# Kernel tuning notes

Hardware: AMD Instinct MI355X
Metric: run time of the kernel (lower is better)

Reference implementation:

```python
import jax, jax.numpy as jnp
import numpy as np

R = 0.2                 # ball-query radius (Descriptor.r)
MAX_NBRS = 64           # CONFIG['Descriptor']['max_num_neighbors']


def setup_inputs() -> dict:
    key = jax.random.key(0)
    k1, k2, k3, k4, k5, k6 = jax.random.split(key, 6)
    N, F, M = 100000, 64, 2048
    x = jax.random.normal(k1, (N, F), dtype=jnp.float32)
    pos = jax.random.normal(k2, (N, 3), dtype=jnp.float32)
    batch = jnp.sort(jax.random.randint(k3, (N,), 0, 4, dtype=jnp.int64))
    key_idx = jax.random.randint(k4, (M,), 0, N, dtype=jnp.int64)
    # MLP params: Linear(F+3 -> 128), ReLU, Linear(128 -> 128)
    H = 128
    W1 = jax.random.normal(k5, (F + 3, H), dtype=jnp.float32) / np.sqrt(F + 3)
    b1 = jnp.zeros((H,), dtype=jnp.float32)
    W2 = jax.random.normal(k6, (H, H), dtype=jnp.float32) / np.sqrt(H)
    b2 = jnp.zeros((H,), dtype=jnp.float32)
    return {"x": x, "pos": pos, "W1": W1, "b1": b1, "W2": W2, "b2": b2,
            "batch": batch, "key_idx": key_idx}


def reference(x, pos, W1, b1, W2, b2, batch, key_idx):
    N = pos.shape[0]
    qpos = pos[key_idx]            # [M,3]
    qbatch = batch[key_idx]        # [M]

    # Brute-force ball query (what torch-cluster radius does under the hood):
    # squared distances via ||q||^2 + ||p||^2 - 2 q.p  -> [M,N]
    d2 = (jnp.sum(qpos * qpos, -1)[:, None]
          + jnp.sum(pos * pos, -1)[None, :]
          - 2.0 * qpos @ pos.T)
    valid = (d2 <= R * R) & (qbatch[:, None] == batch[None, :])   # [M,N]

    # Take the first MAX_NBRS valid neighbors per query (index order, as PyG).
    order_key = jnp.where(valid, jnp.arange(N)[None, :], N)       # invalid -> N
    neg_vals, idx = jax.lax.top_k(-order_key, MAX_NBRS)           # [M,K]
    valid_k = neg_vals > -N                                       # [M,K] real edge mask

    # PointNetConv message: nn(concat([x_j, pos_j - pos_i])), then max-aggregate.
    x_j = x[idx]                                  # [M,K,F] gather
    rel = pos[idx] - qpos[:, None, :]             # [M,K,3]
    h = jnp.concatenate([x_j, rel], axis=-1)      # [M,K,F+3]
    h = jax.nn.relu(h @ W1 + b1)
    h = h @ W2 + b2                               # [M,K,H]
    h = jnp.where(valid_k[..., None], h, -jnp.inf)
    out = jnp.max(h, axis=1)                      # [M,H] max-scatter
    out = jnp.where(jnp.any(valid_k, axis=1)[:, None], out, 0.0)

    # F.normalize(out, dim=-1)
    out = out / jnp.maximum(jnp.linalg.norm(out, axis=-1, keepdims=True), 1e-12)
    return out
```

## Files before the change

### kernel.cpp

```cpp
#include <hip/hip_runtime.h>
#include <math.h>

#define MAXK 64
#define HDIM 128
#define FDIM 64
#define NB 4
#define QG 16
#define S  64

typedef __attribute__((ext_vector_type(8))) short bf16x8;
typedef __attribute__((ext_vector_type(4))) float f32x4;

__device__ __forceinline__ unsigned short f2bf(float f) {
    unsigned x = __float_as_uint(f);
    unsigned r = (x + 0x7fffu + ((x >> 16) & 1u)) >> 16;
    return (unsigned short)r;
}
__device__ __forceinline__ unsigned pk2(float a, float b) {
    return (unsigned)f2bf(a) | ((unsigned)f2bf(b) << 16);
}

__global__ __launch_bounds__(256) void prep_kernel(
    const float* __restrict__ W1, const float* __restrict__ W2,
    const float* __restrict__ pos, const int* __restrict__ batch,
    const int* __restrict__ key_idx, int N, int M,
    unsigned short* __restrict__ W1bf, unsigned short* __restrict__ W2bf,
    float4* __restrict__ posq, int* __restrict__ bounds,
    int* __restrict__ qn, int* __restrict__ qlist)
{
    int t = blockIdx.x * 256 + threadIdx.x;
    if (t < 1536) {
        int s = t;
        int cb = s / 192, rem = s % 192, ks = rem / 64, lane = rem % 64;
        int col = cb*16 + (lane & 15);
        int k0  = ks*32 + (lane >> 4)*8;
        unsigned short v[8];
        #pragma unroll
        for (int j = 0; j < 8; ++j) {
            int k = k0 + j;
            v[j] = (k < 67) ? f2bf(W1[k*HDIM + col]) : (unsigned short)0;
        }
        uint4 p;
        p.x = (unsigned)v[0] | ((unsigned)v[1] << 16);
        p.y = (unsigned)v[2] | ((unsigned)v[3] << 16);
        p.z = (unsigned)v[4] | ((unsigned)v[5] << 16);
        p.w = (unsigned)v[6] | ((unsigned)v[7] << 16);
        *reinterpret_cast<uint4*>(&W1bf[(size_t)s*8]) = p;
    } else if (t < 3584) {
        int s = t - 1536;
        int cb = s >> 8, ks = (s >> 6) & 3, lane = s & 63;
        int col = cb*16 + (lane & 15);
        int k0  = ks*32 + (lane >> 4)*8;
        unsigned short v[8];
        #pragma unroll
        for (int j = 0; j < 8; ++j) v[j] = f2bf(W2[(k0+j)*HDIM + col]);
        uint4 p;
        p.x = (unsigned)v[0] | ((unsigned)v[1] << 16);
        p.y = (unsigned)v[2] | ((unsigned)v[3] << 16);
        p.z = (unsigned)v[4] | ((unsigned)v[5] << 16);
        p.w = (unsigned)v[6] | ((unsigned)v[7] << 16);
        *reinterpret_cast<uint4*>(&W2bf[(size_t)s*8]) = p;
    } else if (t < 3584 + N) {
        int i = t - 3584;
        float px = pos[3*i+0], py = pos[3*i+1], pz = pos[3*i+2];
        float p2 = __fadd_rn(__fadd_rn(__fmul_rn(px,px), __fmul_rn(py,py)), __fmul_rn(pz,pz));
        posq[i] = make_float4(px, py, pz, p2);
    } else if (t < 3584 + 2*N) {
        int i = t - 3584 - N;
        int b1 = batch[i];
        if (i == 0) {
            for (int v = 0; v <= b1; ++v) bounds[v] = 0;
        } else {
            int b0 = batch[i-1];
            for (int v = b0+1; v <= b1; ++v) bounds[v] = i;
        }
        if (i == N-1) {
            for (int v = b1+1; v <= NB; ++v) bounds[v] = N;
        }
    } else if (t < 3584 + 2*N + M) {
        int m = t - 3584 - 2*N;
        int qb = batch[key_idx[m]];
        int slot = atomicAdd(&qn[qb], 1);
        qlist[qb*M + slot] = m;
    }
}

__global__ __launch_bounds__(256) void scan_kernel(
    const float4* __restrict__ posq, const int* __restrict__ key_idx,
    const int* __restrict__ bounds, const int* __restrict__ qn,
    const int* __restrict__ qlist, int M,
    int* __restrict__ lists, int* __restrict__ lcnt)
{
    __shared__ __align__(16) float4 qtile[4][QG];
    __shared__ int qid[4][QG];

    int w = threadIdx.x >> 6, lane = threadIdx.x & 63;
    int unit = blockIdx.x*4 + w;
    int qgidx = unit >> 6, s = unit & (S-1);

    int n0 = qn[0], n1 = qn[1], n2 = qn[2], n3 = qn[3];
    int g0 = (n0+QG-1)/QG, g1 = (n1+QG-1)/QG, g2 = (n2+QG-1)/QG;
    int g3 = (n3+QG-1)/QG;
    int bb, g, nq;
    if      (qgidx < g0)          { bb = 0; g = qgidx;          nq = n0; }
    else if (qgidx < g0+g1)       { bb = 1; g = qgidx-g0;       nq = n1; }
    else if (qgidx < g0+g1+g2)    { bb = 2; g = qgidx-g0-g1;    nq = n2; }
    else if (qgidx < g0+g1+g2+g3) { bb = 3; g = qgidx-g0-g1-g2; nq = n3; }
    else return;

    if (lane < QG) {
        int qs = g*QG + lane;
        int me = (qs < nq) ? qlist[bb*M + qs] : -1;
        qid[w][lane] = me;
        qtile[w][lane] = (me >= 0) ? posq[key_idx[me]] : make_float4(0,0,0,0);
    }

    int lo = bounds[bb], hi = bounds[bb+1];
    int seg  = hi - lo;
    int slen = (seg + S - 1) >> 6;
    int start = lo + s*slen;
    int send  = min(start + slen, hi);

    const float R2 = 0.04f;

    int lc[QG];
    #pragma unroll
    for (int t = 0; t < QG; ++t) lc[t] = (qid[w][t] >= 0) ? 0 : MAXK;

    unsigned long long lmask_lt = (1ull << lane) - 1ull;

    for (int base = start; base < send; base += 64) {
        int j = base + lane;
        float4 p = (j < send) ? posq[j]
                              : make_float4(0.f, 0.f, 0.f, INFINITY);
        #pragma unroll
        for (int t = 0; t < QG; ++t) {
            float4 q = qtile[w][t];
            float dt = __fadd_rn(__fadd_rn(__fmul_rn(q.x,p.x), __fmul_rn(q.y,p.y)), __fmul_rn(q.z,p.z));
            float d2 = __fsub_rn(__fadd_rn(q.w, p.w), __fmul_rn(2.0f, dt));
            bool hit = (d2 <= R2);
            unsigned long long mask = __ballot(hit);
            if (mask) {
                if (hit && lc[t] < MAXK) {
                    int slot = lc[t] + (int)__popcll(mask & lmask_lt);
                    if (slot < MAXK)
                        lists[(qid[w][t]*S + s)*MAXK + slot] = j;
                }
                lc[t] += (int)__popcll(mask);
            }
        }
    }
    #pragma unroll
    for (int t = 0; t < QG; ++t) {
        if (lane == t && qid[w][t] >= 0)
            lcnt[qid[w][t]*S + s] = min(lc[t], MAXK);
    }
}

__global__ __launch_bounds__(256) void mlp_kernel(
    const float* __restrict__ x, const float4* __restrict__ posq,
    const unsigned short* __restrict__ W1bf, const unsigned short* __restrict__ W2bf,
    const float* __restrict__ b1, const float* __restrict__ b2,
    const int* __restrict__ key_idx,
    const int* __restrict__ lists, const int* __restrict__ lcnt,
    float* __restrict__ out, int M)
{
    __shared__ __align__(16) unsigned short h_lds[4*16*128];
    __shared__ float pmax_s[4][HDIM];
    __shared__ float rsum[2];

    int m   = blockIdx.x;
    int tid = threadIdx.x;
    int lane = tid & 63, w = tid >> 6;
    int colq = lane & 15, rq = lane >> 4;

    int qi = key_idx[m];
    float4 q4 = posq[qi];

    int row = w*16 + colq;
    int cnt = 0, src = -1;
    #pragma unroll
    for (int t = 0; t < S; ++t) {
        int ct = lcnt[m*S + t];
        if (row >= cnt && row - cnt < ct) src = (m*S + t)*MAXK + (row - cnt);
        cnt += ct;
    }
    if (cnt > MAXK) cnt = MAXK;

    union { bf16x8 v; uint4 u; } A0, A1, A2;
    A0.u = make_uint4(0,0,0,0); A1.u = A0.u; A2.u = A0.u;
    if (row < cnt) {
        int idx = lists[src];
        const float4* xp = reinterpret_cast<const float4*>(x + (size_t)idx*FDIM + rq*8);
        float4 u0 = xp[0], u1 = xp[1];
        const float4* xq = reinterpret_cast<const float4*>(x + (size_t)idx*FDIM + 32 + rq*8);
        float4 u2 = xq[0], u3 = xq[1];
        A0.u.x = pk2(u0.x, u0.y); A0.u.y = pk2(u0.z, u0.w);
        A0.u.z = pk2(u1.x, u1.y); A0.u.w = pk2(u1.z, u1.w);
        A1.u.x = pk2(u2.x, u2.y); A1.u.y = pk2(u2.z, u2.w);
        A1.u.z = pk2(u3.x, u3.y); A1.u.w = pk2(u3.z, u3.w);
        if (rq == 0) {
            float4 p = posq[idx];
            A2.u.x = pk2(p.x - q4.x, p.y - q4.y);
            A2.u.y = pk2(p.z - q4.z, 0.f);
        }
    }

    const bf16x8* W1f = reinterpret_cast<const bf16x8*>(W1bf);
    const bf16x8* W2f = reinterpret_cast<const bf16x8*>(W2bf);

    #pragma unroll
    for (int cb = 0; cb < 8; ++cb) {
        f32x4 c = {0.f, 0.f, 0.f, 0.f};
        c = __builtin_amdgcn_mfma_f32_16x16x32_bf16(A0.v, W1f[(cb*3+0)*64 + lane], c, 0, 0, 0);
        c = __builtin_amdgcn_mfma_f32_16x16x32_bf16(A1.v, W1f[(cb*3+1)*64 + lane], c, 0, 0, 0);
        c = __builtin_amdgcn_mfma_f32_16x16x32_bf16(A2.v, W1f[(cb*3+2)*64 + lane], c, 0, 0, 0);
        int col = cb*16 + colq;
        float bias = b1[col];
        #pragma unroll
        for (int reg = 0; reg < 4; ++reg) {
            int r = rq*4 + reg;
            float h = fmaxf(c[reg] + bias, 0.f);
            h_lds[w*2048 + r*128 + (col ^ ((r & 7) << 3))] = f2bf(h);
        }
    }

    int r = colq, swz = (r & 7) << 3;
    bf16x8 g0 = *reinterpret_cast<const bf16x8*>(&h_lds[w*2048 + r*128 + ((  0 + rq*8) ^ swz)]);
    bf16x8 g1 = *reinterpret_cast<const bf16x8*>(&h_lds[w*2048 + r*128 + (( 32 + rq*8) ^ swz)]);
    bf16x8 g2 = *reinterpret_cast<const bf16x8*>(&h_lds[w*2048 + r*128 + (( 64 + rq*8) ^ swz)]);
    bf16x8 g3 = *reinterpret_cast<const bf16x8*>(&h_lds[w*2048 + r*128 + (( 96 + rq*8) ^ swz)]);
    #pragma unroll
    for (int cb = 0; cb < 8; ++cb) {
        f32x4 c = {0.f, 0.f, 0.f, 0.f};
        c = __builtin_amdgcn_mfma_f32_16x16x32_bf16(g0, W2f[(cb*4+0)*64 + lane], c, 0, 0, 0);
        c = __builtin_amdgcn_mfma_f32_16x16x32_bf16(g1, W2f[(cb*4+1)*64 + lane], c, 0, 0, 0);
        c = __builtin_amdgcn_mfma_f32_16x16x32_bf16(g2, W2f[(cb*4+2)*64 + lane], c, 0, 0, 0);
        c = __builtin_amdgcn_mfma_f32_16x16x32_bf16(g3, W2f[(cb*4+3)*64 + lane], c, 0, 0, 0);
        int col = cb*16 + colq;
        float bias = b2[col];
        float mx = -INFINITY;
        #pragma unroll
        for (int reg = 0; reg < 4; ++reg) {
            int rr = w*16 + rq*4 + reg;
            float val = c[reg] + bias;
            if (rr < cnt) mx = fmaxf(mx, val);
        }
        mx = fmaxf(mx, __shfl_xor(mx, 16, 64));
        mx = fmaxf(mx, __shfl_xor(mx, 32, 64));
        if (rq == 0) pmax_s[w][col] = mx;
    }
    __syncthreads();

    int c = tid & 127, g = tid >> 7;
    float v = fmaxf(fmaxf(pmax_s[0][c], pmax_s[1][c]),
                    fmaxf(pmax_s[2][c], pmax_s[3][c]));
    if (cnt == 0) v = 0.f;
    float s = (g == 0) ? v*v : 0.f;
    #pragma unroll
    for (int o = 32; o > 0; o >>= 1) s += __shfl_xor(s, o, 64);
    if (g == 0 && (tid & 63) == 0) rsum[tid >> 6] = s;
    __syncthreads();
    if (g == 0) {
        float nrm = fmaxf(sqrtf(rsum[0] + rsum[1]), 1e-12f);
        out[(size_t)m*HDIM + c] = v / nrm;
    }
}

extern "C" void kernel_launch(void* const* d_in, const int* in_sizes, int n_in,
                              void* d_out, int out_size, void* d_ws, size_t ws_size,
                              hipStream_t stream)
{
    const float* x       = (const float*)d_in[0];
    const float* pos     = (const float*)d_in[1];
    const float* W1      = (const float*)d_in[2];
    const float* b1      = (const float*)d_in[3];
    const float* W2      = (const float*)d_in[4];
    const float* b2      = (const float*)d_in[5];
    const int*   batch   = (const int*)d_in[6];
    const int*   key_idx = (const int*)d_in[7];

    int N = in_sizes[6];
    int M = in_sizes[7];

    unsigned short* W1bf = (unsigned short*)d_ws;
    unsigned short* W2bf = W1bf + 12288;
    float4* posq  = (float4*)(W2bf + 16384);
    int* bounds   = (int*)(posq + N);
    int* qn       = bounds + 8;
    int* qlist    = qn + 8;
    int* lists    = qlist + (size_t)NB * M;
    int* lcnt     = lists + (size_t)M * S * MAXK;

    hipMemsetAsync(qn, 0, 8 * sizeof(int), stream);

    int prep_threads = 3584 + 2*N + M;
    prep_kernel<<<(prep_threads + 255)/256, 256, 0, stream>>>(
        W1, W2, pos, batch, key_idx, N, M, W1bf, W2bf, posq, bounds, qn, qlist);

    int max_units = (M/QG + NB) * S;
    scan_kernel<<<(max_units + 3)/4, 256, 0, stream>>>(
        posq, key_idx, bounds, qn, qlist, M, lists, lcnt);

    mlp_kernel<<<M, 256, 0, stream>>>(x, posq, W1bf, W2bf, b1, b2, key_idx,
                                      lists, lcnt, (float*)d_out, M);
}
```

Measured before the change: 148.3 us.

## Shrink prep kernel, drop posq staging, and parallelize MLP neighbor-offset lookup

After: 139.8 us. 5.7% less time.

```diff
diff --git a/kernel.cpp b/kernel.cpp
--- a/kernel.cpp
+++ b/kernel.cpp
@@ -22,77 +22,100 @@
 
 __global__ __launch_bounds__(256) void prep_kernel(
     const float* __restrict__ W1, const float* __restrict__ W2,
-    const float* __restrict__ pos, const int* __restrict__ batch,
-    const int* __restrict__ key_idx, int N, int M,
+    const int* __restrict__ batch, const int* __restrict__ key_idx,
+    int N, int M,
     unsigned short* __restrict__ W1bf, unsigned short* __restrict__ W2bf,
-    float4* __restrict__ posq, int* __restrict__ bounds,
-    int* __restrict__ qn, int* __restrict__ qlist)
+    int* __restrict__ bounds, int* __restrict__ qn, int* __restrict__ qlist)
 {
-    int t = blockIdx.x * 256 + threadIdx.x;
-    if (t < 1536) {
-        int s = t;
-        int cb = s / 192, rem = s % 192, ks = rem / 64, lane = rem % 64;
-        int col = cb*16 + (lane & 15);
-        int k0  = ks*32 + (lane >> 4)*8;
-        unsigned short v[8];
-        #pragma unroll
-        for (int j = 0; j < 8; ++j) {
-            int k = k0 + j;
-            v[j] = (k < 67) ? f2bf(W1[k*HDIM + col]) : (unsigned short)0;
-        }
-        uint4 p;
-        p.x = (unsigned)v[0] | ((unsigned)v[1] << 16);
-        p.y = (unsigned)v[2] | ((unsigned)v[3] << 16);
-        p.z = (unsigned)v[4] | ((unsigned)v[5] << 16);
-        p.w = (unsigned)v[6] | ((unsigned)v[7] << 16);
-        *reinterpret_cast<uint4*>(&W1bf[(size_t)s*8]) = p;
-    } else if (t < 3584) {
-        int s = t - 1536;
-        int cb = s >> 8, ks = (s >> 6) & 3, lane = s & 63;
-        int col = cb*16 + (lane & 15);
-        int k0  = ks*32 + (lane >> 4)*8;
-        unsigned short v[8];
-        #pragma unroll
-        for (int j = 0; j < 8; ++j) v[j] = f2bf(W2[(k0+j)*HDIM + col]);
-        uint4 p;
-        p.x = (unsigned)v[0] | ((unsigned)v[1] << 16);
-        p.y = (unsigned)v[2] | ((unsigned)v[3] << 16);
-        p.z = (unsigned)v[4] | ((unsigned)v[5] << 16);
-        p.w = (unsigned)v[6] | ((unsigned)v[7] << 16);
-        *reinterpret_cast<uint4*>(&W2bf[(size_t)s*8]) = p;
-    } else if (t < 3584 + N) {
-        int i = t - 3584;
-        float px = pos[3*i+0], py = pos[3*i+1], pz = pos[3*i+2];
-        float p2 = __fadd_rn(__fadd_rn(__fmul_rn(px,px), __fmul_rn(py,py)), __fmul_rn(pz,pz));
-        posq[i] = make_float4(px, py, pz, p2);
-    } else if (t < 3584 + 2*N) {
-        int i = t - 3584 - N;
-        int b1 = batch[i];
-        if (i == 0) {
-            for (int v = 0; v <= b1; ++v) bounds[v] = 0;
-        } else {
-            int b0 = batch[i-1];
-            for (int v = b0+1; v <= b1; ++v) bounds[v] = i;
-        }
-        if (i == N-1) {
-            for (int v = b1+1; v <= NB; ++v) bounds[v] = N;
-        }
-    } else if (t < 3584 + 2*N + M) {
-        int m = t - 3584 - 2*N;
-        int qb = batch[key_idx[m]];
-        int slot = atomicAdd(&qn[qb], 1);
-        qlist[qb*M + slot] = m;
+    int tid = threadIdx.x;
+    if (blockIdx.x == 0) {
+        __shared__ int wcnt[4][NB];
+        __shared__ int base[NB];
+        int lane = tid & 63, w = tid >> 6;
+        if (tid < NB) base[tid] = 0;
+        __syncthreads();
+        int nchunk = (M + 255) / 256;
+        for (int c = 0; c < nchunk; ++c) {
+            int i = c*256 + tid;
+            int qb = (i < M) ? batch[key_idx[i]] : -1;
+            unsigned long long m0 = __ballot(qb == 0);
+            unsigned long long m1 = __ballot(qb == 1);
+            unsigned long long m2 = __ballot(qb == 2);
+            unsigned long long m3 = __ballot(qb == 3);
+            if (lane == 0) {
+                wcnt[w][0] = (int)__popcll(m0); wcnt[w][1] = (int)__popcll(m1);
+                wcnt[w][2] = (int)__popcll(m2); wcnt[w][3] = (int)__popcll(m3);
+            }
+            __syncthreads();
+            if (qb >= 0) {
+                unsigned long long mym = (qb == 0) ? m0 : (qb == 1) ? m1
+                                        : (qb == 2) ? m2 : m3;
+                int off = 0;
+                for (int ww = 0; ww < 4; ++ww)
+                    if (ww < w) off += wcnt[ww][qb];
+                int slot = base[qb] + off
+                         + (int)__popcll(mym & ((1ull << lane) - 1ull));
+                qlist[qb*M + slot] = i;
+            }
+            __syncthreads();
+            if (tid < NB) {
+                int t2 = 0;
+                for (int ww = 0; ww < 4; ++ww) t2 += wcnt[ww][tid];
+                base[tid] += t2;
+            }
+            __syncthreads();
+        }
+        if (tid < NB) qn[tid] = base[tid];
+    } else if (blockIdx.x == 1) {
+        if (tid <= NB) {
+            int v = tid, a = 0, e = N;
+            while (a < e) { int mid = (a+e) >> 1; if (batch[mid] < v) a = mid+1; else e = mid; }
+            bounds[v] = a;
+        }
+    } else {
+        int s = (blockIdx.x - 2)*256 + tid;
+        if (s < 1536) {
+            int cb = s / 192, rem = s % 192, ks = rem / 64, lane = rem % 64;
+            int col = cb*16 + (lane & 15);
+            int k0  = ks*32 + (lane >> 4)*8;
+            unsigned short v[8];
+            #pragma unroll
+            for (int j = 0; j < 8; ++j) {
+                int k = k0 + j;
+                v[j] = (k < 67) ? f2bf(W1[k*HDIM + col]) : (unsigned short)0;
+            }
+            uint4 p;
+            p.x = (unsigned)v[0] | ((unsigned)v[1] << 16);
+            p.y = (unsigned)v[2] | ((unsigned)v[3] << 16);
+            p.z = (unsigned)v[4] | ((unsigned)v[5] << 16);
+            p.w = (unsigned)v[6] | ((unsigned)v[7] << 16);
+            *reinterpret_cast<uint4*>(&W1bf[(size_t)s*8]) = p;
+        } else if (s < 3584) {
+            int s2 = s - 1536;
+            int cb = s2 >> 8, ks = (s2 >> 6) & 3, lane = s2 & 63;
+            int col = cb*16 + (lane & 15);
+            int k0  = ks*32 + (lane >> 4)*8;
+            unsigned short v[8];
+            #pragma unroll
+            for (int j = 0; j < 8; ++j) v[j] = f2bf(W2[(k0+j)*HDIM + col]);
+            uint4 p;
+            p.x = (unsigned)v[0] | ((unsigned)v[1] << 16);
+            p.y = (unsigned)v[2] | ((unsigned)v[3] << 16);
+            p.z = (unsigned)v[4] | ((unsigned)v[5] << 16);
+            p.w = (unsigned)v[6] | ((unsigned)v[7] << 16);
+            *reinterpret_cast<uint4*>(&W2bf[(size_t)s2*8]) = p;
+        }
     }
 }
 
 __global__ __launch_bounds__(256) void scan_kernel(
-    const float4* __restrict__ posq, const int* __restrict__ key_idx,
+    const float* __restrict__ pos, const int* __restrict__ key_idx,
     const int* __restrict__ bounds, const int* __restrict__ qn,
     const int* __restrict__ qlist, int M,
     int* __restrict__ lists, int* __restrict__ lcnt)
 {
     __shared__ __align__(16) float4 qtile[4][QG];
-    __shared__ int qid[4][QG];
+    __shared__ int qid_s[4][QG];
 
     int w = threadIdx.x >> 6, lane = threadIdx.x & 63;
     int unit = blockIdx.x*4 + w;
@@ -111,9 +134,19 @@
     if (lane < QG) {
         int qs = g*QG + lane;
         int me = (qs < nq) ? qlist[bb*M + qs] : -1;
-        qid[w][lane] = me;
-        qtile[w][lane] = (me >= 0) ? posq[key_idx[me]] : make_float4(0,0,0,0);
-    }
+        qid_s[w][lane] = me;
+        float4 qv = make_float4(0.f, 0.f, 0.f, 0.f);
+        if (me >= 0) {
+            int qi = key_idx[me];
+            float qx = pos[3*qi+0], qy = pos[3*qi+1], qz = pos[3*qi+2];
+            float q2 = __fadd_rn(__fadd_rn(__fmul_rn(qx,qx), __fmul_rn(qy,qy)), __fmul_rn(qz,qz));
+            qv = make_float4(qx, qy, qz, q2);
+        }
+        qtile[w][lane] = qv;
+    }
+    float4 qr[QG]; int qidr[QG];
+    #pragma unroll
+    for (int t = 0; t < QG; ++t) { qr[t] = qtile[w][t]; qidr[t] = qid_s[w][t]; }
 
     int lo = bounds[bb], hi = bounds[bb+1];
     int seg  = hi - lo;
@@ -125,26 +158,31 @@
 
     int lc[QG];
     #pragma unroll
-    for (int t = 0; t < QG; ++t) lc[t] = (qid[w][t] >= 0) ? 0 : MAXK;
+    for (int t = 0; t < QG; ++t) lc[t] = (qidr[t] >= 0) ? 0 : MAXK;
 
     unsigned long long lmask_lt = (1ull << lane) - 1ull;
 
     for (int base = start; base < send; base += 64) {
         int j = base + lane;
-        float4 p = (j < send) ? posq[j]
-                              : make_float4(0.f, 0.f, 0.f, INFINITY);
+        float px, py, pz, pw;
+        if (j < send) {
+            px = pos[3*j+0]; py = pos[3*j+1]; pz = pos[3*j+2];
+            pw = __fadd_rn(__fadd_rn(__fmul_rn(px,px), __fmul_rn(py,py)), __fmul_rn(pz,pz));
+        } else {
+            px = 0.f; py = 0.f; pz = 0.f; pw = INFINITY;
+        }
         #pragma unroll
         for (int t = 0; t < QG; ++t) {
-            float4 q = qtile[w][t];
-            float dt = __fadd_rn(__fadd_rn(__fmul_rn(q.x,p.x), __fmul_rn(q.y,p.y)), __fmul_rn(q.z,p.z));
-            float d2 = __fsub_rn(__fadd_rn(q.w, p.w), __fmul_rn(2.0f, dt));
+            float4 q = qr[t];
+            float dt = __fadd_rn(__fadd_rn(__fmul_rn(q.x,px), __fmul_rn(q.y,py)), __fmul_rn(q.z,pz));
+            float d2 = __fsub_rn(__fadd_rn(q.w, pw), __fmul_rn(2.0f, dt));
             bool hit = (d2 <= R2);
             unsigned long long mask = __ballot(hit);
             if (mask) {
                 if (hit && lc[t] < MAXK) {
                     int slot = lc[t] + (int)__popcll(mask & lmask_lt);
                     if (slot < MAXK)
-                        lists[(qid[w][t]*S + s)*MAXK + slot] = j;
+                        lists[(qidr[t]*S + s)*MAXK + slot] = j;
                 }
                 lc[t] += (int)__popcll(mask);
             }
@@ -152,13 +190,13 @@
     }
     #pragma unroll
     for (int t = 0; t < QG; ++t) {
-        if (lane == t && qid[w][t] >= 0)
-            lcnt[qid[w][t]*S + s] = min(lc[t], MAXK);
+        if (lane == t && qidr[t] >= 0)
+            lcnt[qidr[t]*S + s] = min(lc[t], MAXK);
     }
 }
 
 __global__ __launch_bounds__(256) void mlp_kernel(
-    const float* __restrict__ x, const float4* __restrict__ posq,
+    const float* __restrict__ x, const float* __restrict__ pos,
     const unsigned short* __restrict__ W1bf, const unsigned short* __restrict__ W2bf,
     const float* __restrict__ b1, const float* __restrict__ b2,
     const int* __restrict__ key_idx,
@@ -175,17 +213,29 @@
     int colq = lane & 15, rq = lane >> 4;
 
     int qi = key_idx[m];
-    float4 q4 = posq[qi];
+    float qx = pos[3*qi+0], qy = pos[3*qi+1], qz = pos[3*qi+2];
+
+    int ct = lcnt[m*S + lane];
+    int pre = ct;
+    #pragma unroll
+    for (int o = 1; o < 64; o <<= 1) {
+        int v = __shfl_up(pre, o, 64);
+        if (lane >= o) pre += v;
+    }
+    int excl = pre - ct;
+    int total = __shfl(pre, 63, 64);
+    int cnt = min(total, MAXK);
 
     int row = w*16 + colq;
-    int cnt = 0, src = -1;
-    #pragma unroll
-    for (int t = 0; t < S; ++t) {
-        int ct = lcnt[m*S + t];
-        if (row >= cnt && row - cnt < ct) src = (m*S + t)*MAXK + (row - cnt);
-        cnt += ct;
-    }
-    if (cnt > MAXK) cnt = MAXK;
+    int sp = 0;
+    #pragma unroll
+    for (int st = 32; st >= 1; st >>= 1) {
+        int cand = sp + st;
+        int e = __shfl(excl, (cand < 64) ? cand : 63, 64);
+        if (cand < 64 && e <= row) sp = cand;
+    }
+    int off = row - __shfl(excl, sp, 64);
+    int src = (m*S + sp)*MAXK + off;
 
     union { bf16x8 v; uint4 u; } A0, A1, A2;
     A0.u = make_uint4(0,0,0,0); A1.u = A0.u; A2.u = A0.u;
@@ -200,9 +250,9 @@
         A1.u.x = pk2(u2.x, u2.y); A1.u.y = pk2(u2.z, u2.w);
         A1.u.z = pk2(u3.x, u3.y); A1.u.w = pk2(u3.z, u3.w);
         if (rq == 0) {
-            float4 p = posq[idx];
-            A2.u.x = pk2(p.x - q4.x, p.y - q4.y);
-            A2.u.y = pk2(p.z - q4.z, 0.f);
+            float p0 = pos[3*idx+0], p1 = pos[3*idx+1], p2v = pos[3*idx+2];
+            A2.u.x = pk2(p0 - qx, p1 - qy);
+            A2.u.y = pk2(p2v - qz, 0.f);
         }
     }
 
@@ -256,10 +306,10 @@
     float v = fmaxf(fmaxf(pmax_s[0][c], pmax_s[1][c]),
                     fmaxf(pmax_s[2][c], pmax_s[3][c]));
     if (cnt == 0) v = 0.f;
-    float s = (g == 0) ? v*v : 0.f;
-    #pragma unroll
-    for (int o = 32; o > 0; o >>= 1) s += __shfl_xor(s, o, 64);
-    if (g == 0 && (tid & 63) == 0) rsum[tid >> 6] = s;
+    float sacc = (g == 0) ? v*v : 0.f;
+    #pragma unroll
+    for (int o = 32; o > 0; o >>= 1) sacc += __shfl_xor(sacc, o, 64);
+    if (g == 0 && (tid & 63) == 0) rsum[tid >> 6] = sacc;
     __syncthreads();
     if (g == 0) {
         float nrm = fmaxf(sqrtf(rsum[0] + rsum[1]), 1e-12f);
@@ -285,23 +335,19 @@
 
     unsigned short* W1bf = (unsigned short*)d_ws;
     unsigned short* W2bf = W1bf + 12288;
-    float4* posq  = (float4*)(W2bf + 16384);
-    int* bounds   = (int*)(posq + N);
+    int* bounds   = (int*)(W2bf + 16384);
     int* qn       = bounds + 8;
     int* qlist    = qn + 8;
     int* lists    = qlist + (size_t)NB * M;
     int* lcnt     = lists + (size_t)M * S * MAXK;
 
-    hipMemsetAsync(qn, 0, 8 * sizeof(int), stream);
-
-    int prep_threads = 3584 + 2*N + M;
-    prep_kernel<<<(prep_threads + 255)/256, 256, 0, stream>>>(
-        W1, W2, pos, batch, key_idx, N, M, W1bf, W2bf, posq, bounds, qn, qlist);
+    prep_kernel<<<16, 256, 0, stream>>>(W1, W2, batch, key_idx, N, M,
+                                        W1bf, W2bf, bounds, qn, qlist);
 
     int max_units = (M/QG + NB) * S;
     scan_kernel<<<(max_units + 3)/4, 256, 0, stream>>>(
-        posq, key_idx, bounds, qn, qlist, M, lists, lcnt);
-
-    mlp_kernel<<<M, 256, 0, stream>>>(x, posq, W1bf, W2bf, b1, b2, key_idx,
+        pos, key_idx, bounds, qn, qlist, M, lists, lcnt);
+
+    mlp_kernel<<<M, 256, 0, stream>>>(x, pos, W1bf, W2bf, b1, b2, key_idx,
                                       lists, lcnt, (float*)d_out, M);
 }
```
